# Performance work log

Measured on AMD Instinct MI355X. Metric: run time of the kernel, lower is better.

Reference implementation:

```python
import jax, jax.numpy as jnp
import numpy as np

NUM_GRIDS = 16
IN_X, IN_Z, OUT, BATCH = 32, 32, 64, 512


def _borders_cdf_grid(n_chunks):
    def inv_cdf(u):
        return np.log(2.0 * u) if u <= 0.5 else -np.log(2.0 * (1.0 - u))
    cs = 1.0 / n_chunks
    b = [inv_cdf(i * cs) for i in range(1, n_chunks)]
    left = b[0] - (b[1] - b[0])
    right = b[-1] + (b[-1] - b[-2])
    return np.array([left] + b + [right], dtype=np.float32)


def _laplace_cdf(v):
    e = jnp.exp(-jnp.abs(v))
    return jnp.where(v > 0, 1.0 - 0.5 * e, 0.5 * e)


def setup_inputs() -> dict:
    key = jax.random.key(0)
    k1, k2, k3 = jax.random.split(key, 3)
    scale = 0.1 / np.sqrt(IN_X * IN_Z)
    borders_np = _borders_cdf_grid(NUM_GRIDS)
    inv_len_np = (1.0 / (borders_np[1:] - borders_np[:-1])).astype(np.float32)
    return {
        "x": jax.random.normal(k1, (IN_X, BATCH), dtype=jnp.float32),
        "z": jax.random.normal(k2, (IN_Z, BATCH), dtype=jnp.float32),
        "func_parameter": jax.random.uniform(
            k3, (NUM_GRIDS + 1, NUM_GRIDS + 1, OUT, IN_X, IN_Z),
            dtype=jnp.float32, minval=-scale, maxval=scale),
        "borders": jnp.asarray(borders_np),
        "inverse_chunk_lengths": jnp.asarray(inv_len_np[:NUM_GRIDS]),
    }


def reference(x, z, func_parameter, borders, inverse_chunk_lengths):
    G = inverse_chunk_lengths.shape[0]
    Ix, B = x.shape
    Iz = z.shape[0]

    # data-dependent bin indices per (input_dim, batch) element
    idx_x = jnp.clip((_laplace_cdf(x) * G).astype(jnp.int32), 0, G - 1)  # [Ix,B]
    idx_z = jnp.clip((_laplace_cdf(z) * G).astype(jnp.int32), 0, G - 1)  # [Iz,B]
    dx = (x - borders[idx_x]) * inverse_chunk_lengths[idx_x]             # [Ix,B]
    dz = (z - borders[idx_z]) * inverse_chunk_lengths[idx_z]             # [Iz,B]
    idx_xn = jnp.clip(idx_x + 1, 0, G)
    idx_zn = jnp.clip(idx_z + 1, 0, G)

    # [Ix, Iz, G+1, G+1, O] so the per-(ix,iz) tables are leading-indexed
    Pt = jnp.transpose(func_parameter, (3, 4, 0, 1, 2))
    ax = jnp.arange(Ix)[:, None, None]   # [Ix,1,1]
    az = jnp.arange(Iz)[None, :, None]   # [1,Iz,1]

    def corner(ii, jj):  # ii:[Ix,1,B] or broadcastable, jj:[1,Iz,B]
        return Pt[ax, az, ii, jj]        # -> [Ix,Iz,B,O]

    ixb, ixnb = idx_x[:, None, :], idx_xn[:, None, :]
    izb, iznb = idx_z[None, :, :], idx_zn[None, :, :]
    wx, wz = dx[:, None, :], dz[None, :, :]             # [Ix,1,B],[1,Iz,B]

    out = (
        jnp.einsum('xzb,xzbo->ob', (1 - wx) * (1 - wz), corner(ixb, izb))
        + jnp.einsum('xzb,xzbo->ob', (1 - wx) * wz, corner(ixb, iznb))
        + jnp.einsum('xzb,xzbo->ob', wx * (1 - wz), corner(ixnb, izb))
        + jnp.einsum('xzb,xzbo->ob', wx * wz, corner(ixnb, iznb))
    )
    return out  # [output_dim, batch]
```

## Files before the change

kernel.cpp:

```cpp
#include <hip/hip_runtime.h>


#define NG        16
#define NB        17
#define IN_X      32
#define IN_Z      32
#define OUT_DIM   64
#define BATCH     512
#define CELLS     (NB * NB)
#define LDS_STR   33
#define XSTR      (NB * LDS_STR)

__device__ __forceinline__ void grid_coord(float v,
                                           const float* __restrict__ borders,
                                           const float* __restrict__ inv_len,
                                           int& idx, float& w) {
    float e   = expf(-fabsf(v));
    float cdf = (v > 0.f) ? (1.f - 0.5f * e) : (0.5f * e);
    int t = (int)(cdf * 16.f);
    t = t < 0 ? 0 : (t > NG - 1 ? NG - 1 : t);
    idx = t;
    w = (v - borders[t]) * inv_len[t];
}

__device__ __forceinline__ unsigned pack_bf16(float a, float b) {
    unsigned ua = __float_as_uint(a);
    unsigned ub = __float_as_uint(b);
    ua += 0x7FFFu + ((ua >> 16) & 1u);
    ub += 0x7FFFu + ((ub >> 16) & 1u);
    return (ua >> 16) | (ub & 0xFFFF0000u);
}

__device__ __forceinline__ float bf_lo(unsigned u) {
    return __uint_as_float(u << 16);
}
__device__ __forceinline__ float bf_hi(unsigned u) {
    return __uint_as_float(u & 0xFFFF0000u);
}

__global__ void precompute_kernel(const float* __restrict__ x,
                                  const float* __restrict__ z,
                                  const float* __restrict__ borders,
                                  const float* __restrict__ inv_len,
                                  float2* __restrict__ xc,
                                  float2* __restrict__ zc,
                                  float* __restrict__ out) {
    const int gid = blockIdx.x * blockDim.x + threadIdx.x;
    out[gid] = 0.f;
    int idx; float w;
    if (gid < IN_X * BATCH) {
        grid_coord(x[gid], borders, inv_len, idx, w);
        xc[gid] = make_float2(w, __int_as_float(idx * XSTR));
    } else {
        const int g = gid - IN_X * BATCH;
        grid_coord(z[g], borders, inv_len, idx, w);
        zc[g] = make_float2(w, __int_as_float(idx * LDS_STR));
    }
}

__global__ __launch_bounds__(512, 8)
void bf2d_kernel(const float2* __restrict__ xc,
                 const float2* __restrict__ zc,
                 const float* __restrict__ P,
                 float* __restrict__ out) {
    __shared__ unsigned lds[CELLS * LDS_STR];

    const int tid = threadIdx.x;
    const int o0  = (blockIdx.x & 31) * 2;
    const int i   = blockIdx.x >> 5;

    const float* Pbase = P + ((size_t)o0 * (IN_X * IN_Z) + (size_t)i * IN_Z);
    for (int k = tid; k < CELLS * IN_Z; k += 512) {
        const int c = k >> 5;
        const int j = k & 31;
        const size_t g = (size_t)c * (OUT_DIM * IN_X * IN_Z) + j;
        lds[c * LDS_STR + j] = pack_bf16(Pbase[g], Pbase[g + IN_X * IN_Z]);
    }
    __syncthreads();

    const float2 xcv  = xc[i * BATCH + tid];
    const float  wx   = xcv.x;
    const int    xoff = __float_as_int(xcv.y);

    const float2* zp = zc + tid;
    float accx = 0.f, accy = 0.f;
    #pragma unroll 4
    for (int j = 0; j < IN_Z; ++j) {
        const float2 zcv = zp[j * BATCH];
        const float  wz  = zcv.x;
        const int    base = xoff + __float_as_int(zcv.y) + j;
        const unsigned a0 = lds[base];
        const unsigned a1 = lds[base + LDS_STR];
        const unsigned b0 = lds[base + XSTR];
        const unsigned b1 = lds[base + XSTR + LDS_STR];
        const float lox = bf_lo(a0) + wz * (bf_lo(a1) - bf_lo(a0));
        const float loy = bf_hi(a0) + wz * (bf_hi(a1) - bf_hi(a0));
        const float hix = bf_lo(b0) + wz * (bf_lo(b1) - bf_lo(b0));
        const float hiy = bf_hi(b0) + wz * (bf_hi(b1) - bf_hi(b0));
        accx += lox + wx * (hix - lox);
        accy += loy + wx * (hiy - loy);
    }

    atomicAdd(&out[o0 * BATCH + tid],       accx);
    atomicAdd(&out[(o0 + 1) * BATCH + tid], accy);
}

extern "C" void kernel_launch(void* const* d_in, const int* in_sizes, int n_in,
                              void* d_out, int out_size, void* d_ws, size_t ws_size,
                              hipStream_t stream) {
    const float* x       = (const float*)d_in[0];
    const float* z       = (const float*)d_in[1];
    const float* P       = (const float*)d_in[2];
    const float* borders = (const float*)d_in[3];
    const float* inv_len = (const float*)d_in[4];
    float* out = (float*)d_out;

    float2* xc = (float2*)d_ws;
    float2* zc = xc + IN_X * BATCH;

    precompute_kernel<<<dim3(128), dim3(256), 0, stream>>>(
        x, z, borders, inv_len, xc, zc, out);

    bf2d_kernel<<<dim3((OUT_DIM / 2) * IN_X), dim3(512), 0, stream>>>(
        xc, zc, P, out);
}
```

Measured before the change: 123.4 us.

## Process four x-rows per block with vectorized float4 table staging

Restructures the main kernel so each 1024-thread block handles four input-x rows for an output pair, staging a larger bf16 LDS table via float4 global loads. Each thread processes two x rows per batch element, sharing z-coordinate loads and halving atomics per output. The grid shrinks to 256 blocks with ~154KB LDS each, trading cross-block latency hiding and occupancy for fewer, wider loads.

Measured after the change: 122.2 us. No clear change (-0.9%).

```diff
diff --git a/kernel.cpp b/kernel.cpp
--- a/kernel.cpp
+++ b/kernel.cpp
@@ -8,8 +8,10 @@
 #define OUT_DIM   64
 #define BATCH     512
 #define CELLS     (NB * NB)
-#define LDS_STR   33
-#define XSTR      (NB * LDS_STR)
+#define CSTRIDE   133
+#define ILSTRIDE  33
+#define XSTR_A    (NB * CSTRIDE)
+#define STASKS    (CELLS * 32)
 
 __device__ __forceinline__ void grid_coord(float v,
                                            const float* __restrict__ borders,
@@ -30,7 +32,6 @@
     ub += 0x7FFFu + ((ub >> 16) & 1u);
     return (ua >> 16) | (ub & 0xFFFF0000u);
 }
-
 __device__ __forceinline__ float bf_lo(unsigned u) {
     return __uint_as_float(u << 16);
 }
@@ -43,66 +44,100 @@
                                   const float* __restrict__ borders,
                                   const float* __restrict__ inv_len,
                                   float2* __restrict__ xc,
-                                  float2* __restrict__ zc,
+                                  uint2* __restrict__ zc,
                                   float* __restrict__ out) {
     const int gid = blockIdx.x * blockDim.x + threadIdx.x;
     out[gid] = 0.f;
     int idx; float w;
     if (gid < IN_X * BATCH) {
         grid_coord(x[gid], borders, inv_len, idx, w);
-        xc[gid] = make_float2(w, __int_as_float(idx * XSTR));
+        xc[gid] = make_float2(w, __int_as_float(idx * XSTR_A));
     } else {
         const int g = gid - IN_X * BATCH;
         grid_coord(z[g], borders, inv_len, idx, w);
-        zc[g] = make_float2(w, __int_as_float(idx * LDS_STR));
+        zc[g] = make_uint2(__float_as_uint(w), (unsigned)(idx * CSTRIDE));
     }
 }
 
-__global__ __launch_bounds__(512, 8)
+__global__ __launch_bounds__(1024, 1)
 void bf2d_kernel(const float2* __restrict__ xc,
-                 const float2* __restrict__ zc,
+                 const uint2* __restrict__ zc,
                  const float* __restrict__ P,
                  float* __restrict__ out) {
-    __shared__ unsigned lds[CELLS * LDS_STR];
+    __shared__ unsigned lds[CELLS * CSTRIDE];
 
     const int tid = threadIdx.x;
-    const int o0  = (blockIdx.x & 31) * 2;
-    const int i   = blockIdx.x >> 5;
+    const int op  = blockIdx.x & 31;
+    const int iq  = blockIdx.x >> 5;
+    const int o0  = op * 2;
 
-    const float* Pbase = P + ((size_t)o0 * (IN_X * IN_Z) + (size_t)i * IN_Z);
-    for (int k = tid; k < CELLS * IN_Z; k += 512) {
-        const int c = k >> 5;
-        const int j = k & 31;
-        const size_t g = (size_t)c * (OUT_DIM * IN_X * IN_Z) + j;
-        lds[c * LDS_STR + j] = pack_bf16(Pbase[g], Pbase[g + IN_X * IN_Z]);
+    const float* Pb = P + (size_t)o0 * 1024 + iq * 128;
+    #pragma unroll
+    for (int it = 0; it < 10; ++it) {
+        const int k = tid + it * 1024;
+        if (k < STASKS) {
+            const int c  = k >> 5;
+            const int f4 = k & 31;
+            const float* g = Pb + (size_t)c * 65536 + f4 * 4;
+            const float4 a = *(const float4*)g;
+            const float4 b = *(const float4*)(g + 1024);
+            unsigned* d = &lds[c * CSTRIDE + (f4 >> 3) * ILSTRIDE
+                               + ((f4 & 7) << 2)];
+            d[0] = pack_bf16(a.x, b.x);
+            d[1] = pack_bf16(a.y, b.y);
+            d[2] = pack_bf16(a.z, b.z);
+            d[3] = pack_bf16(a.w, b.w);
+        }
     }
     __syncthreads();
 
-    const float2 xcv  = xc[i * BATCH + tid];
-    const float  wx   = xcv.x;
-    const int    xoff = __float_as_int(xcv.y);
+    const int b  = tid & (BATCH - 1);
+    const int ih = tid >> 9;
+    const int il0 = 2 * ih, il1 = 2 * ih + 1;
 
-    const float2* zp = zc + tid;
+    const float2 x0 = xc[(iq * 4 + il0) * BATCH + b];
+    const float2 x1 = xc[(iq * 4 + il1) * BATCH + b];
+    const float wx0 = x0.x, wx1 = x1.x;
+    const int   xo0 = __float_as_int(x0.y) + il0 * ILSTRIDE;
+    const int   xo1 = __float_as_int(x1.y) + il1 * ILSTRIDE;
+
+    const uint2* zp = zc + b;
     float accx = 0.f, accy = 0.f;
     #pragma unroll 4
     for (int j = 0; j < IN_Z; ++j) {
-        const float2 zcv = zp[j * BATCH];
-        const float  wz  = zcv.x;
-        const int    base = xoff + __float_as_int(zcv.y) + j;
-        const unsigned a0 = lds[base];
-        const unsigned a1 = lds[base + LDS_STR];
-        const unsigned b0 = lds[base + XSTR];
-        const unsigned b1 = lds[base + XSTR + LDS_STR];
-        const float lox = bf_lo(a0) + wz * (bf_lo(a1) - bf_lo(a0));
-        const float loy = bf_hi(a0) + wz * (bf_hi(a1) - bf_hi(a0));
-        const float hix = bf_lo(b0) + wz * (bf_lo(b1) - bf_lo(b0));
-        const float hiy = bf_hi(b0) + wz * (bf_hi(b1) - bf_hi(b0));
-        accx += lox + wx * (hix - lox);
-        accy += loy + wx * (hiy - loy);
+        const uint2 zv = zp[j * BATCH];
+        const float wz = __uint_as_float(zv.x);
+        const int   zo = (int)zv.y + j;
+        {
+            const int base = xo0 + zo;
+            const unsigned a0 = lds[base];
+            const unsigned a1 = lds[base + CSTRIDE];
+            const unsigned b0 = lds[base + XSTR_A];
+            const unsigned b1 = lds[base + XSTR_A + CSTRIDE];
+            const float lox = bf_lo(a0) + wz * (bf_lo(a1) - bf_lo(a0));
+            const float loy = bf_hi(a0) + wz * (bf_hi(a1) - bf_hi(a0));
+            const float hix = bf_lo(b0) + wz * (bf_lo(b1) - bf_lo(b0));
+            const float hiy = bf_hi(b0) + wz * (bf_hi(b1) - bf_hi(b0));
+            accx += lox + wx0 * (hix - lox);
+            accy += loy + wx0 * (hiy - loy);
+        }
+        {
+            const int base = xo1 + zo;
+            const unsigned a0 = lds[base];
+            const unsigned a1 = lds[base + CSTRIDE];
+            const unsigned b0 = lds[base + XSTR_A];
+            const unsigned b1 = lds[base + XSTR_A + CSTRIDE];
+            const float lox = bf_lo(a0) + wz * (bf_lo(a1) - bf_lo(a0));
+            const float loy = bf_hi(a0) + wz * (bf_hi(a1) - bf_hi(a0));
+            const float hix = bf_lo(b0) + wz * (bf_lo(b1) - bf_lo(b0));
+            const float hiy = bf_hi(b0) + wz * (bf_hi(b1) - bf_hi(b0));
+            accx += lox + wx1 * (hix - lox);
+            accy += loy + wx1 * (hiy - loy);
+        }
     }
 
-    atomicAdd(&out[o0 * BATCH + tid],       accx);
-    atomicAdd(&out[(o0 + 1) * BATCH + tid], accy);
+    atomicAdd(&out[o0 * BATCH + b],       accx);
+    atomicAdd(&out[(o0 + 1) * BATCH + b], accy);
 }
 
 extern "C" void kernel_launch(void* const* d_in, const int* in_sizes, int n_in,
@@ -116,11 +151,10 @@
     float* out = (float*)d_out;
 
     float2* xc = (float2*)d_ws;
-    float2* zc = xc + IN_X * BATCH;
+    uint2*  zc = (uint2*)(xc + IN_X * BATCH);
 
     precompute_kernel<<<dim3(128), dim3(256), 0, stream>>>(
         x, z, borders, inv_len, xc, zc, out);
 
-    bf2d_kernel<<<dim3((OUT_DIM / 2) * IN_X), dim3(512), 0, stream>>>(
-        xc, zc, P, out);
+    bf2d_kernel<<<dim3(32 * 8), dim3(1024), 0, stream>>>(xc, zc, P, out);
 }
```
